# Kernel tuning notes

Measured on AMD Instinct MI355X. Metric: run time of the kernel, lower is better.

## Reference

```python
import jax, jax.numpy as jnp
import numpy as np
from jax import lax

V, E, H, D = 50000, 300, 128, 128   # vocab, embed, gru_units, dense_units
B, S, W, T = 32, 512, 20, 16        # batch, sentences/doc, words/sentence, topics/doc


def setup_inputs() -> dict:
    key = jax.random.key(0)
    ks = jax.random.split(key, 16)
    word_ids = jax.random.randint(ks[0], (B, S, W), 0, V, dtype=jnp.int32)
    # contiguous equal topic segments, 1-based inclusive boundaries
    L = S // T
    starts = (1 + np.arange(T) * L).astype(np.int32)
    ends = (starts + L - 1).astype(np.int32)
    topic_start_ends = jnp.asarray(np.broadcast_to(np.stack([starts, ends], -1), (B, T, 2)))
    sc = 0.05
    def rn(k, shape, s=sc):
        return jax.random.normal(k, shape, dtype=jnp.float32) * s
    inp = {
        "word_ids": word_ids,
        "topic_start_ends": topic_start_ends,
        "emb": rn(ks[1], (V, E), 0.6),
        "Wih_f": rn(ks[2], (3 * H, E)), "Whh_f": rn(ks[3], (3 * H, H)),
        "bih_f": rn(ks[4], (3 * H,)),   "bhh_f": rn(ks[5], (3 * H,)),
        "Wih_b": rn(ks[6], (3 * H, E)), "Whh_b": rn(ks[7], (3 * H, H)),
        "bih_b": rn(ks[8], (3 * H,)),   "bhh_b": rn(ks[9], (3 * H,)),
        "W_att": rn(ks[10], (4 * H, 4 * H)), "v_att": rn(ks[11], (4 * H, 1)),
        "W1": rn(ks[12], (D, 4 * H)), "b1": rn(ks[13], (D,)),
        "W2": rn(ks[14], (1, D)),     "b2": rn(ks[15], (1,)),
    }
    return inp


def _gru_dir(x_sbe, Wih, Whh, bih, bhh, reverse):
    """x_sbe: [S,B,E] -> (outputs [S,B,H] in original time order, last hidden [B,H])."""
    h0 = jnp.zeros((x_sbe.shape[1], Whh.shape[1]), x_sbe.dtype)
    def step(h, xt):
        gx = xt @ Wih.T + bih            # [B,3H]
        gh = h @ Whh.T + bhh
        xr, xz, xn = jnp.split(gx, 3, axis=-1)   # PyTorch gate order: r,z,n
        hr, hz, hn = jnp.split(gh, 3, axis=-1)
        r = jax.nn.sigmoid(xr + hr)
        z = jax.nn.sigmoid(xz + hz)
        n = jnp.tanh(xn + r * hn)
        h2 = (1.0 - z) * n + z * h
        return h2, h2
    last, outs = lax.scan(step, h0, x_sbe, reverse=reverse)
    return outs, last


def reference(word_ids, topic_start_ends, emb,
              Wih_f, Whh_f, bih_f, bhh_f,
              Wih_b, Whh_b, bih_b, bhh_b,
              W_att, v_att, W1, b1, W2, b2):
    # --- sent_encoder: mean word embedding per sentence ---
    x = jnp.mean(emb[word_ids], axis=2)              # [B,S,E]
    # --- doc_encoder: biGRU over sentences ---
    xs = jnp.swapaxes(x, 0, 1)                       # [S,B,E]
    out_f, last_f = _gru_dir(xs, Wih_f, Whh_f, bih_f, bhh_f, reverse=False)
    out_b, last_b = _gru_dir(xs, Wih_b, Whh_b, bih_b, bhh_b, reverse=True)
    sent_rep = jnp.swapaxes(jnp.concatenate([out_f, out_b], axis=-1), 0, 1)  # [B,S,2H]
    # faithful to torch hidden.view(B, 2H) on [2,B,H] contiguous memory
    doc_vec = jnp.stack([last_f, last_b], axis=0).reshape(sent_rep.shape[0], 2 * last_f.shape[1])
    doc_rep = jnp.broadcast_to(doc_vec[:, None, :], sent_rep.shape)          # [B,S,2H]
    # --- topic segment extraction via boundary diffs on zero-padded GRU out ---
    Bn, Sn, twoH = sent_rep.shape
    Hn = twoH // 2
    P = jnp.pad(sent_rep, ((0, 0), (1, 1), (0, 0)))   # [B,S+2,2H]; index i = 1-based sentence i
    starts = topic_start_ends[..., 0]                 # [B,T], 1-based
    ends = topic_start_ends[..., 1]
    bidx = jnp.arange(Bn)[:, None]
    fw = P[bidx, ends, :Hn] - P[bidx, starts - 1, :Hn]      # forward-dir diff
    bw = P[bidx, starts, Hn:] - P[bidx, ends + 1, Hn:]      # backward-dir diff
    topic_mat = jnp.concatenate([fw, bw], axis=-1)          # [B,T,2H]
    # scatter: sentence s (0-based) belongs to topic with starts-1 <= s <= ends-1
    pos = jnp.arange(Sn, dtype=starts.dtype) + 1            # 1-based sentence ids
    seg = jax.vmap(lambda st: jnp.searchsorted(st, pos, side='right') - 1)(starts)  # [B,S]
    topic_rep = jnp.take_along_axis(topic_mat, seg[..., None], axis=1)              # [B,S,2H]
    # --- decoder ---
    cat_ds = jnp.concatenate([doc_rep, sent_rep], axis=-1)   # [B,S,4H]
    cat_ts = jnp.concatenate([topic_rep, sent_rep], axis=-1)
    doc_scores = jnp.tanh(cat_ds @ W_att) @ v_att            # [B,S,1]
    topic_scores = jnp.tanh(cat_ts @ W_att) @ v_att
    ssum = doc_scores + topic_scores
    context = (doc_scores / ssum) * doc_rep + (topic_scores / ssum) * topic_rep
    inp = jnp.concatenate([sent_rep, context], axis=-1)      # [B,S,4H]
    h = jax.nn.relu(inp @ W1.T + b1)                         # dropout = identity (eval)
    logits = h @ W2.T + b2                                   # [B,S,1]
    return logits
```

## Files before the change

kernel.cpp:

```cpp
#include <hip/hip_runtime.h>
#include <hip/hip_bf16.h>

#define B_ 32
#define S_ 512
#define W_ 20
#define T_ 16
#define E_ 300
#define H_ 128
#define M_ (B_*S_)

#define OFF_GX        0ul
#define OFF_X         12582912ul
#define OFF_SENT      17498112ul
#define OFF_LASTF     21692416ul
#define OFF_LASTB     21696512ul
#define OFF_DOCVEC    21700608ul
#define OFF_TOPICMAT  21708800ul
#define OFF_DOCPART   21839872ul
#define OFF_TOPICPART 21856256ul
#define OFF_SEG       22118400ul
#define OFF_WTIH      22134784ul
#define OFF_BIASIH    22365184ul
#define OFF_W1T       22365952ul
#define OFF_H         22431488ul
#define OFF_SRPART    0ul
#define OFF_CTX       OFF_X

__global__ void prep_kernel(const float* __restrict__ Wih_f, const float* __restrict__ Wih_b,
                            const float* __restrict__ bih_f, const float* __restrict__ bih_b,
                            const float* __restrict__ W1,
                            float* __restrict__ Wt_ih, float* __restrict__ bias_ih,
                            float* __restrict__ W1t) {
  int idx = blockIdx.x * 256 + threadIdx.x;
  if (idx < E_ * 768) {
    int k = idx / 768, g = idx % 768;
    Wt_ih[idx] = (g < 384) ? Wih_f[g * E_ + k] : Wih_b[(g - 384) * E_ + k];
  }
  if (idx < 768) bias_ih[idx] = (idx < 384) ? bih_f[idx] : bih_b[idx - 384];
  if (idx < 512 * 128) { int k = idx / 128, j = idx % 128; W1t[idx] = W1[j * 512 + k]; }
}

__global__ void embed_mean_kernel(const int* __restrict__ wid, const float* __restrict__ emb,
                                  float* __restrict__ x) {
  int m = blockIdx.x;
  const int* ids = wid + (size_t)m * W_;
  int e = threadIdx.x;
  float s0 = 0.f, s1 = 0.f, s2 = 0.f;
  for (int w = 0; w < W_; w++) {
    const float* row = emb + (size_t)ids[w] * E_;
    s0 += row[e];
    s1 += row[e + 128];
    if (e < E_ - 256) s2 += row[e + 256];
  }
  const float inv = 1.0f / (float)W_;
  float* xr = x + (size_t)m * E_;
  xr[e] = s0 * inv; xr[e + 128] = s1 * inv; if (e < E_ - 256) xr[e + 256] = s2 * inv;
}

template<bool BIAS, bool ACCUM, bool RELU>
__global__ __launch_bounds__(256) void gemm64(
    const float* __restrict__ A, int lda,
    const float* __restrict__ B, int ldb,
    float* __restrict__ C, int ldc,
    const float* __restrict__ bias,
    int M, int N, int K) {
  __shared__ float As[16][68];
  __shared__ float Bs[16][68];
  const int tid = threadIdx.x;
  const int n0 = blockIdx.x * 64, m0 = blockIdx.y * 64;
  const int tx = tid & 15, ty = tid >> 4;
  const int am = tid >> 2, ak = (tid & 3) << 2;
  const int bk = tid >> 4, bn = (tid & 15) << 2;
  float acc[4][4] = {};
  for (int k0 = 0; k0 < K; k0 += 16) {
    float4 av = make_float4(0.f, 0.f, 0.f, 0.f);
    int arow = m0 + am;
    if (arow < M) {
      if (k0 + ak + 3 < K) {
        av = *(const float4*)(A + (size_t)arow * lda + k0 + ak);
      } else {
        float tmp[4] = {0.f, 0.f, 0.f, 0.f};
        #pragma unroll
        for (int i2 = 0; i2 < 4; i2++) { int k = k0 + ak + i2; if (k < K) tmp[i2] = A[(size_t)arow * lda + k]; }
        av = make_float4(tmp[0], tmp[1], tmp[2], tmp[3]);
      }
    }
    As[ak + 0][am] = av.x; As[ak + 1][am] = av.y; As[ak + 2][am] = av.z; As[ak + 3][am] = av.w;
    float4 bv = make_float4(0.f, 0.f, 0.f, 0.f);
    {
      int k = k0 + bk;
      if (k < K) bv = *(const float4*)(B + (size_t)k * ldb + n0 + bn);
    }
    *(float4*)&Bs[bk][bn] = bv;
    __syncthreads();
    #pragma unroll
    for (int kk = 0; kk < 16; kk++) {
      float4 a = *(const float4*)&As[kk][ty << 2];
      float4 b = *(const float4*)&Bs[kk][tx << 2];
      acc[0][0] = fmaf(a.x, b.x, acc[0][0]); acc[0][1] = fmaf(a.x, b.y, acc[0][1]);
      acc[0][2] = fmaf(a.x, b.z, acc[0][2]); acc[0][3] = fmaf(a.x, b.w, acc[0][3]);
      acc[1][0] = fmaf(a.y, b.x, acc[1][0]); acc[1][1] = fmaf(a.y, b.y, acc[1][1]);
      acc[1][2] = fmaf(a.y, b.z, acc[1][2]); acc[1][3] = fmaf(a.y, b.w, acc[1][3]);
      acc[2][0] = fmaf(a.z, b.x, acc[2][0]); acc[2][1] = fmaf(a.z, b.y, acc[2][1]);
      acc[2][2] = fmaf(a.z, b.z, acc[2][2]); acc[2][3] = fmaf(a.z, b.w, acc[2][3]);
      acc[3][0] = fmaf(a.w, b.x, acc[3][0]); acc[3][1] = fmaf(a.w, b.y, acc[3][1]);
      acc[3][2] = fmaf(a.w, b.z, acc[3][2]); acc[3][3] = fmaf(a.w, b.w, acc[3][3]);
    }
    __syncthreads();
  }
  float4 bias4 = make_float4(0.f, 0.f, 0.f, 0.f);
  if (BIAS) bias4 = *(const float4*)(bias + n0 + (tx << 2));
  #pragma unroll
  for (int i = 0; i < 4; i++) {
    int row = m0 + (ty << 2) + i;
    if (row >= M) break;
    float* cp = C + (size_t)row * ldc + n0 + (tx << 2);
    float4 v = make_float4(acc[i][0], acc[i][1], acc[i][2], acc[i][3]);
    if (BIAS) { v.x += bias4.x; v.y += bias4.y; v.z += bias4.z; v.w += bias4.w; }
    if (ACCUM) { float4 o = *(const float4*)cp; v.x += o.x; v.y += o.y; v.z += o.z; v.w += o.w; }
    if (RELU) { v.x = fmaxf(v.x, 0.f); v.y = fmaxf(v.y, 0.f); v.z = fmaxf(v.z, 0.f); v.w = fmaxf(v.w, 0.f); }
    *(float4*)cp = v;
  }
}

__global__ __launch_bounds__(384, 2) void gru_kernel(
    const float* __restrict__ gxbuf,
    const float* __restrict__ Whh_f, const float* __restrict__ Whh_b,
    const float* __restrict__ bhh_f, const float* __restrict__ bhh_b,
    float* __restrict__ sent_rep,
    float* __restrict__ last_f, float* __restrict__ last_b) {
  int bid = blockIdx.x;
  int dir = bid >> 5, b = bid & 31;
  int g = threadIdx.x;
  const float* Whh = dir ? Whh_b : Whh_f;
  const float* bhh = dir ? bhh_b : bhh_f;
  float4 w[32];
  #pragma unroll
  for (int kk = 0; kk < 32; kk++) w[kk] = *(const float4*)(Whh + (size_t)g * 128 + kk * 4);
  float bh = bhh[g];
  __shared__ float h_lds[128];
  __shared__ float r_lds[128];
  __shared__ float z_lds[128];
  if (g < 128) h_lds[g] = 0.f;
  __syncthreads();
  int j = g - 256;
  const float* gx0 = gxbuf + (size_t)b * 512 * 768 + dir * 384 + g;
  int ts = dir ? 511 : 0;
  int step = dir ? -1 : 1;
  float* srow = sent_rep + (size_t)b * 512 * 256 + dir * 128;
  float gx_c = gx0[(size_t)ts * 768];
  float gx_n1 = gx0[(size_t)(ts + step) * 768];
  for (int s = 0; s < 512; s++) {
    float gx_n2 = 0.f;
    if (s + 2 < 512) gx_n2 = gx0[(size_t)(ts + 2 * step) * 768];
    float4 acc4 = make_float4(0.f, 0.f, 0.f, 0.f);
    const float4* h4 = (const float4*)h_lds;
    #pragma unroll
    for (int kk = 0; kk < 32; kk++) {
      float4 hv = h4[kk];
      acc4.x = fmaf(w[kk].x, hv.x, acc4.x);
      acc4.y = fmaf(w[kk].y, hv.y, acc4.y);
      acc4.z = fmaf(w[kk].z, hv.z, acc4.z);
      acc4.w = fmaf(w[kk].w, hv.w, acc4.w);
    }
    float hdot = (acc4.x + acc4.y) + (acc4.z + acc4.w) + bh;
    if (g < 256) {
      float pre = gx_c + hdot;
      float sg_ = 1.f / (1.f + expf(-pre));
      if (g < 128) r_lds[g] = sg_; else z_lds[g - 128] = sg_;
    }
    __syncthreads();
    if (g >= 256) {
      float r = r_lds[j];
      float nval = tanhf(gx_c + r * hdot);
      float z = z_lds[j];
      float hold = h_lds[j];
      float hnew = (1.f - z) * nval + z * hold;
      h_lds[j] = hnew;
      srow[(size_t)ts * 256 + j] = hnew;
    }
    __syncthreads();
    ts += step;
    gx_c = gx_n1; gx_n1 = gx_n2;
  }
  if (g < 128) (dir ? last_b : last_f)[b * 128 + g] = h_lds[g];
}

__global__ void docvec_kernel(const float* __restrict__ last_f, const float* __restrict__ last_b,
                              float* __restrict__ doc_vec) {
  int idx = blockIdx.x * 256 + threadIdx.x;
  int i = idx >> 8, c = idx & 255;
  const float* src = (i < 16) ? last_f : last_b;
  int ii = (i < 16) ? i : i - 16;
  int bb = 2 * ii + (c >> 7);
  doc_vec[idx] = src[bb * 128 + (c & 127)];
}

__global__ void topicmat_kernel(const float* __restrict__ sent_rep, const int* __restrict__ tse,
                                float* __restrict__ topic_mat) {
  int bt = blockIdx.x;
  int b = bt >> 4, t = bt & 15;
  int st = tse[(b * 16 + t) * 2 + 0];
  int en = tse[(b * 16 + t) * 2 + 1];
  int jj = threadIdx.x;
  const float* sr = sent_rep + (size_t)b * 512 * 256;
  float val;
  if (jj < 128) {
    float a = sr[(size_t)(en - 1) * 256 + jj];
    float c = (st - 2 >= 0) ? sr[(size_t)(st - 2) * 256 + jj] : 0.f;
    val = a - c;
  } else {
    float a = sr[(size_t)(st - 1) * 256 + jj];
    float c = (en <= 511) ? sr[(size_t)en * 256 + jj] : 0.f;
    val = a - c;
  }
  topic_mat[(size_t)bt * 256 + jj] = val;
}

__global__ void seg_kernel(const int* __restrict__ tse, int* __restrict__ seg) {
  int idx = blockIdx.x * 256 + threadIdx.x;
  int b = idx >> 9, s = idx & 511;
  int pos = s + 1, cnt = 0;
  for (int t = 0; t < T_; t++) cnt += (tse[(b * T_ + t) * 2] <= pos);
  int sg = cnt - 1; sg = sg < 0 ? 0 : (sg > T_ - 1 ? T_ - 1 : sg);
  seg[idx] = sg;
}

__global__ void scores_ctx_kernel(const float* __restrict__ sr_part,
                                  const float* __restrict__ doc_part,
                                  const float* __restrict__ topic_part,
                                  const float* __restrict__ v_att,
                                  const float* __restrict__ doc_vec,
                                  const float* __restrict__ topic_mat,
                                  const int* __restrict__ seg,
                                  float* __restrict__ context) {
  int wid = threadIdx.x >> 6, lane = threadIdx.x & 63;
  int row = blockIdx.x * 4 + wid;
  int b = row >> 9;
  int sg = seg[row];
  const float* srp = sr_part + (size_t)row * 512;
  const float* dp = doc_part + (size_t)b * 512;
  const float* tp = topic_part + (size_t)(b * 16 + sg) * 512;
  float accd = 0.f, acct = 0.f;
  #pragma unroll
  for (int i = 0; i < 8; i++) {
    int n = lane + i * 64;
    float sp = srp[n], va = v_att[n];
    accd += tanhf(dp[n] + sp) * va;
    acct += tanhf(tp[n] + sp) * va;
  }
  #pragma unroll
  for (int off = 32; off; off >>= 1) { accd += __shfl_xor(accd, off); acct += __shfl_xor(acct, off); }
  float ssum = accd + acct;
  float rd = accd / ssum, rt = acct / ssum;
  const float* dv = doc_vec + (size_t)b * 256;
  const float* tm = topic_mat + (size_t)(b * 16 + sg) * 256;
  float* ctx = context + (size_t)row * 256;
  #pragma unroll
  for (int i = 0; i < 4; i++) {
    int jj = lane + i * 64;
    ctx[jj] = rd * dv[jj] + rt * tm[jj];
  }
}

__global__ void logits_kernel(const float* __restrict__ h, const float* __restrict__ W2,
                              const float* __restrict__ b2, float* __restrict__ out, int M) {
  int wid = threadIdx.x >> 6, lane = threadIdx.x & 63;
  int row = blockIdx.x * 4 + wid;
  if (row >= M) return;
  const float* hp = h + (size_t)row * 128;
  float s = hp[lane] * W2[lane] + hp[lane + 64] * W2[lane + 64];
  #pragma unroll
  for (int off = 32; off; off >>= 1) s += __shfl_xor(s, off);
  if (lane == 0) out[row] = s + b2[0];
}

extern "C" void kernel_launch(void* const* d_in, const int* in_sizes, int n_in,
                              void* d_out, int out_size, void* d_ws, size_t ws_size,
                              hipStream_t stream) {
  const int*   word_ids = (const int*)d_in[0];
  const int*   tse      = (const int*)d_in[1];
  const float* emb      = (const float*)d_in[2];
  const float* Wih_f    = (const float*)d_in[3];
  const float* Whh_f    = (const float*)d_in[4];
  const float* bih_f    = (const float*)d_in[5];
  const float* bhh_f    = (const float*)d_in[6];
  const float* Wih_b    = (const float*)d_in[7];
  const float* Whh_b    = (const float*)d_in[8];
  const float* bih_b    = (const float*)d_in[9];
  const float* bhh_b    = (const float*)d_in[10];
  const float* W_att    = (const float*)d_in[11];
  const float* v_att    = (const float*)d_in[12];
  const float* W1       = (const float*)d_in[13];
  const float* b1       = (const float*)d_in[14];
  const float* W2       = (const float*)d_in[15];
  const float* b2       = (const float*)d_in[16];
  float* ws  = (float*)d_ws;
  float* out = (float*)d_out;

  prep_kernel<<<900, 256, 0, stream>>>(Wih_f, Wih_b, bih_f, bih_b, W1,
                                       ws + OFF_WTIH, ws + OFF_BIASIH, ws + OFF_W1T);
  embed_mean_kernel<<<M_, 128, 0, stream>>>(word_ids, emb, ws + OFF_X);
  gemm64<true, false, false><<<dim3(12, 256), 256, 0, stream>>>(
      ws + OFF_X, E_, ws + OFF_WTIH, 768, ws + OFF_GX, 768, ws + OFF_BIASIH, M_, 768, E_);
  gru_kernel<<<64, 384, 0, stream>>>(ws + OFF_GX, Whh_f, Whh_b, bhh_f, bhh_b,
                                     ws + OFF_SENT, ws + OFF_LASTF, ws + OFF_LASTB);
  docvec_kernel<<<32, 256, 0, stream>>>(ws + OFF_LASTF, ws + OFF_LASTB, ws + OFF_DOCVEC);
  topicmat_kernel<<<512, 256, 0, stream>>>(ws + OFF_SENT, tse, ws + OFF_TOPICMAT);
  seg_kernel<<<64, 256, 0, stream>>>(tse, (int*)(ws + OFF_SEG));
  gemm64<false, false, false><<<dim3(8, 1), 256, 0, stream>>>(
      ws + OFF_DOCVEC, 256, W_att, 512, ws + OFF_DOCPART, 512, nullptr, 32, 512, 256);
  gemm64<false, false, false><<<dim3(8, 8), 256, 0, stream>>>(
      ws + OFF_TOPICMAT, 256, W_att, 512, ws + OFF_TOPICPART, 512, nullptr, 512, 512, 256);
  gemm64<false, false, false><<<dim3(8, 256), 256, 0, stream>>>(
      ws + OFF_SENT, 256, W_att + 256 * 512, 512, ws + OFF_SRPART, 512, nullptr, M_, 512, 256);
  scores_ctx_kernel<<<M_ / 4, 256, 0, stream>>>(
      ws + OFF_SRPART, ws + OFF_DOCPART, ws + OFF_TOPICPART, v_att,
      ws + OFF_DOCVEC, ws + OFF_TOPICMAT, (const int*)(ws + OFF_SEG), ws + OFF_CTX);
  gemm64<true, false, false><<<dim3(2, 256), 256, 0, stream>>>(
      ws + OFF_SENT, 256, ws + OFF_W1T, 128, ws + OFF_H, 128, b1, M_, 128, 256);
  gemm64<false, true, true><<<dim3(2, 256), 256, 0, stream>>>(
      ws + OFF_CTX, 256, ws + OFF_W1T + 256 * 128, 128, ws + OFF_H, 128, nullptr, M_, 128, 256);
  logits_kernel<<<M_ / 4, 256, 0, stream>>>(ws + OFF_H, W2, b2, out, M_);
}
```

Before: 842.7 us.

## Restructure GRU recurrence as split-K across waves with readlane hidden-state broadcast

The GRU recurrent kernel now uses 256 threads per block. Each thread computes all three gates for one hidden unit over half of the K dimension, taking h values from registers via readlane broadcasts instead of reading them from LDS. Owner threads keep h in a register, add the partial sums from the other half, and apply the gate nonlinearities. This removes LDS reads of h from the inner loop and shortens the serial path per timestep, at the cost of 192 weight registers per thread and a partial-sum exchange through shared memory.

```diff
diff --git a/kernel.cpp b/kernel.cpp
--- a/kernel.cpp
+++ b/kernel.cpp
@@ -123,67 +123,88 @@
   }
 }
 
-__global__ __launch_bounds__(384, 2) void gru_kernel(
+__global__ __launch_bounds__(256, 1) void gru_kernel(
     const float* __restrict__ gxbuf,
     const float* __restrict__ Whh_f, const float* __restrict__ Whh_b,
     const float* __restrict__ bhh_f, const float* __restrict__ bhh_b,
     float* __restrict__ sent_rep,
     float* __restrict__ last_f, float* __restrict__ last_b) {
-  int bid = blockIdx.x;
-  int dir = bid >> 5, b = bid & 31;
-  int g = threadIdx.x;
+  const int bid = blockIdx.x;
+  const int dir = bid >> 5, b = bid & 31;
+  const int t = threadIdx.x;
+  const int j = t & 127;
+  const int lane = t & 63;
+  const int q = ((t >> 6) ^ (t >> 7)) & 1;
+  const int k0 = q << 6;
+  const bool owner = (t < 128);
   const float* Whh = dir ? Whh_b : Whh_f;
   const float* bhh = dir ? bhh_b : bhh_f;
-  float4 w[32];
-  #pragma unroll
-  for (int kk = 0; kk < 32; kk++) w[kk] = *(const float4*)(Whh + (size_t)g * 128 + kk * 4);
-  float bh = bhh[g];
-  __shared__ float h_lds[128];
-  __shared__ float r_lds[128];
-  __shared__ float z_lds[128];
-  if (g < 128) h_lds[g] = 0.f;
+
+  float wr[64], wz[64], wn[64];
+  #pragma unroll
+  for (int kk = 0; kk < 64; kk += 4) {
+    float4 a = *(const float4*)(Whh + (size_t)j * 128 + k0 + kk);
+    wr[kk] = a.x; wr[kk + 1] = a.y; wr[kk + 2] = a.z; wr[kk + 3] = a.w;
+    float4 c = *(const float4*)(Whh + (size_t)(128 + j) * 128 + k0 + kk);
+    wz[kk] = c.x; wz[kk + 1] = c.y; wz[kk + 2] = c.z; wz[kk + 3] = c.w;
+    float4 d = *(const float4*)(Whh + (size_t)(256 + j) * 128 + k0 + kk);
+    wn[kk] = d.x; wn[kk + 1] = d.y; wn[kk + 2] = d.z; wn[kk + 3] = d.w;
+  }
+  float bhr = 0.f, bhz = 0.f, bhn = 0.f;
+  if (owner) { bhr = bhh[j]; bhz = bhh[128 + j]; bhn = bhh[256 + j]; }
+
+  __shared__ float hbuf[128];
+  __shared__ float rp[128], zp[128], np_[128];
+  if (t < 128) hbuf[t] = 0.f;
   __syncthreads();
-  int j = g - 256;
-  const float* gx0 = gxbuf + (size_t)b * 512 * 768 + dir * 384 + g;
+
+  float hown = 0.f;
+  const float* gx0 = gxbuf + (size_t)b * 512 * 768 + dir * 384 + j;
   int ts = dir ? 511 : 0;
-  int step = dir ? -1 : 1;
+  const int stp = dir ? -1 : 1;
   float* srow = sent_rep + (size_t)b * 512 * 256 + dir * 128;
-  float gx_c = gx0[(size_t)ts * 768];
-  float gx_n1 = gx0[(size_t)(ts + step) * 768];
+
+  float gr_c = 0.f, gz_c = 0.f, gn_c = 0.f, gr_1 = 0.f, gz_1 = 0.f, gn_1 = 0.f;
+  if (owner) {
+    const float* p0 = gx0 + (size_t)ts * 768;
+    gr_c = p0[0]; gz_c = p0[128]; gn_c = p0[256];
+    const float* p1 = gx0 + (size_t)(ts + stp) * 768;
+    gr_1 = p1[0]; gz_1 = p1[128]; gn_1 = p1[256];
+  }
+
   for (int s = 0; s < 512; s++) {
-    float gx_n2 = 0.f;
-    if (s + 2 < 512) gx_n2 = gx0[(size_t)(ts + 2 * step) * 768];
-    float4 acc4 = make_float4(0.f, 0.f, 0.f, 0.f);
-    const float4* h4 = (const float4*)h_lds;
+    float gr_2 = 0.f, gz_2 = 0.f, gn_2 = 0.f;
+    if (owner && s + 2 < 512) {
+      const float* p2 = gx0 + (size_t)(ts + 2 * stp) * 768;
+      gr_2 = p2[0]; gz_2 = p2[128]; gn_2 = p2[256];
+    }
+    float hreg = owner ? hown : hbuf[k0 + lane];
+    float ar = 0.f, az = 0.f, an = 0.f;
     #pragma unroll
-    for (int kk = 0; kk < 32; kk++) {
-      float4 hv = h4[kk];
-      acc4.x = fmaf(w[kk].x, hv.x, acc4.x);
-      acc4.y = fmaf(w[kk].y, hv.y, acc4.y);
-      acc4.z = fmaf(w[kk].z, hv.z, acc4.z);
-      acc4.w = fmaf(w[kk].w, hv.w, acc4.w);
-    }
-    float hdot = (acc4.x + acc4.y) + (acc4.z + acc4.w) + bh;
-    if (g < 256) {
-      float pre = gx_c + hdot;
-      float sg_ = 1.f / (1.f + expf(-pre));
-      if (g < 128) r_lds[g] = sg_; else z_lds[g - 128] = sg_;
-    }
+    for (int kk = 0; kk < 64; kk++) {
+      float hv = __int_as_float(__builtin_amdgcn_readlane(__float_as_int(hreg), kk));
+      ar = fmaf(wr[kk], hv, ar);
+      az = fmaf(wz[kk], hv, az);
+      an = fmaf(wn[kk], hv, an);
+    }
+    if (!owner) { rp[j] = ar; zp[j] = az; np_[j] = an; }
     __syncthreads();
-    if (g >= 256) {
-      float r = r_lds[j];
-      float nval = tanhf(gx_c + r * hdot);
-      float z = z_lds[j];
-      float hold = h_lds[j];
-      float hnew = (1.f - z) * nval + z * hold;
-      h_lds[j] = hnew;
+    if (owner) {
+      ar += rp[j]; az += zp[j]; an += np_[j];
+      float r = 1.f / (1.f + expf(-(gr_c + ar + bhr)));
+      float z = 1.f / (1.f + expf(-(gz_c + az + bhz)));
+      float n = tanhf(gn_c + r * (an + bhn));
+      float hnew = (1.f - z) * n + z * hown;
+      hown = hnew;
+      hbuf[j] = hnew;
       srow[(size_t)ts * 256 + j] = hnew;
     }
     __syncthreads();
-    ts += step;
-    gx_c = gx_n1; gx_n1 = gx_n2;
-  }
-  if (g < 128) (dir ? last_b : last_f)[b * 128 + g] = h_lds[g];
+    ts += stp;
+    gr_c = gr_1; gz_c = gz_1; gn_c = gn_1;
+    gr_1 = gr_2; gz_1 = gz_2; gn_1 = gn_2;
+  }
+  if (owner) (dir ? last_b : last_f)[b * 128 + j] = hown;
 }
 
 __global__ void docvec_kernel(const float* __restrict__ last_f, const float* __restrict__ last_b,
@@ -303,7 +324,7 @@
   embed_mean_kernel<<<M_, 128, 0, stream>>>(word_ids, emb, ws + OFF_X);
   gemm64<true, false, false><<<dim3(12, 256), 256, 0, stream>>>(
       ws + OFF_X, E_, ws + OFF_WTIH, 768, ws + OFF_GX, 768, ws + OFF_BIASIH, M_, 768, E_);
-  gru_kernel<<<64, 384, 0, stream>>>(ws + OFF_GX, Whh_f, Whh_b, bhh_f, bhh_b,
+  gru_kernel<<<64, 256, 0, stream>>>(ws + OFF_GX, Whh_f, Whh_b, bhh_f, bhh_b,
                                      ws + OFF_SENT, ws + OFF_LASTF, ws + OFF_LASTB);
   docvec_kernel<<<32, 256, 0, stream>>>(ws + OFF_LASTF, ws + OFF_LASTB, ws + OFF_DOCVEC);
   topicmat_kernel<<<512, 256, 0, stream>>>(ws + OFF_SENT, tse, ws + OFF_TOPICMAT);
```

New measurement: 935.3 us. +11.0%, slower.

## Restructure GRU recurrence into split-K wave layout with one barrier per step

Applied to the files above, without the earlier changes.

The GRU recurrence kernel now uses 512 threads per block. Each hidden unit's r, z and n dot products are split across four 16-lane groups, each covering 32 of the 128 inputs, and the partial sums are combined with cross-lane shuffles. This lets each thread compute all three gates for its unit in registers, and double-buffering the hidden state in LDS cuts the per-step barriers from two to one. The serial 512-step loop is the critical path, so removing a barrier and the LDS round trips for r and z should shorten each step, at the cost of shuffle reductions and tighter register pressure from the pinned weights.

```diff
diff --git a/kernel.cpp b/kernel.cpp
--- a/kernel.cpp
+++ b/kernel.cpp
@@ -123,67 +123,89 @@
   }
 }
 
-__global__ __launch_bounds__(384, 2) void gru_kernel(
+#define PIN4(v) asm volatile("" : "+v"((v).x), "+v"((v).y), "+v"((v).z), "+v"((v).w))
+__global__ __launch_bounds__(512) __attribute__((amdgpu_waves_per_eu(2, 2)))
+void gru_kernel(
     const float* __restrict__ gxbuf,
     const float* __restrict__ Whh_f, const float* __restrict__ Whh_b,
     const float* __restrict__ bhh_f, const float* __restrict__ bhh_b,
     float* __restrict__ sent_rep,
     float* __restrict__ last_f, float* __restrict__ last_b) {
-  int bid = blockIdx.x;
-  int dir = bid >> 5, b = bid & 31;
-  int g = threadIdx.x;
+  const int bid = blockIdx.x;
+  const int dir = bid >> 5, b = bid & 31;
+  const int t = threadIdx.x;
+  const int wave = t >> 6;
+  const int lane = t & 63;
+  const int q = lane >> 4;
+  const int j = (wave << 4) + (lane & 15);
+  const int k0 = q << 5;
   const float* Whh = dir ? Whh_b : Whh_f;
   const float* bhh = dir ? bhh_b : bhh_f;
-  float4 w[32];
-  #pragma unroll
-  for (int kk = 0; kk < 32; kk++) w[kk] = *(const float4*)(Whh + (size_t)g * 128 + kk * 4);
-  float bh = bhh[g];
-  __shared__ float h_lds[128];
-  __shared__ float r_lds[128];
-  __shared__ float z_lds[128];
-  if (g < 128) h_lds[g] = 0.f;
+
+  float4 wr4[8], wz4[8], wn4[8];
+  #pragma unroll
+  for (int i = 0; i < 8; i++) {
+    wr4[i] = *(const float4*)(Whh + (size_t)j * 128 + k0 + i * 4);
+    wz4[i] = *(const float4*)(Whh + (size_t)(128 + j) * 128 + k0 + i * 4);
+    wn4[i] = *(const float4*)(Whh + (size_t)(256 + j) * 128 + k0 + i * 4);
+  }
+  #pragma unroll
+  for (int i = 0; i < 8; i++) { PIN4(wr4[i]); PIN4(wz4[i]); PIN4(wn4[i]); }
+
+  const float bhr = bhh[j], bhz = bhh[128 + j], bhn = bhh[256 + j];
+  const int gate = q ? (q - 1) : 2;
+  const float mr = (q == 1) ? 1.f : 0.f;
+  const float mz = (q == 2) ? 1.f : 0.f;
+  const float* gxp = gxbuf + (size_t)b * 512 * 768 + dir * 384 + gate * 128 + j;
+
+  __shared__ float hbuf[2][128];
+  if (t < 128) hbuf[0][t] = 0.f;
   __syncthreads();
-  int j = g - 256;
-  const float* gx0 = gxbuf + (size_t)b * 512 * 768 + dir * 384 + g;
+
+  float hprev = 0.f;
   int ts = dir ? 511 : 0;
-  int step = dir ? -1 : 1;
+  const int stp = dir ? -1 : 1;
   float* srow = sent_rep + (size_t)b * 512 * 256 + dir * 128;
-  float gx_c = gx0[(size_t)ts * 768];
-  float gx_n1 = gx0[(size_t)(ts + step) * 768];
+
+  float gx_c = gxp[(size_t)ts * 768];
+  float gx_1 = gxp[(size_t)(ts + stp) * 768];
+
+  #pragma unroll 1
   for (int s = 0; s < 512; s++) {
-    float gx_n2 = 0.f;
-    if (s + 2 < 512) gx_n2 = gx0[(size_t)(ts + 2 * step) * 768];
-    float4 acc4 = make_float4(0.f, 0.f, 0.f, 0.f);
-    const float4* h4 = (const float4*)h_lds;
+    float gx_2 = 0.f;
+    if (s + 2 < 512) gx_2 = gxp[(size_t)(ts + 2 * stp) * 768];
+    const float4* h4 = (const float4*)(&hbuf[s & 1][k0]);
+    float pr = 0.f, pz = 0.f, pn = 0.f;
     #pragma unroll
-    for (int kk = 0; kk < 32; kk++) {
-      float4 hv = h4[kk];
-      acc4.x = fmaf(w[kk].x, hv.x, acc4.x);
-      acc4.y = fmaf(w[kk].y, hv.y, acc4.y);
-      acc4.z = fmaf(w[kk].z, hv.z, acc4.z);
-      acc4.w = fmaf(w[kk].w, hv.w, acc4.w);
-    }
-    float hdot = (acc4.x + acc4.y) + (acc4.z + acc4.w) + bh;
-    if (g < 256) {
-      float pre = gx_c + hdot;
-      float sg_ = 1.f / (1.f + expf(-pre));
-      if (g < 128) r_lds[g] = sg_; else z_lds[g - 128] = sg_;
+    for (int i = 0; i < 8; i++) {
+      float4 hv = h4[i];
+      pr = fmaf(wr4[i].x, hv.x, pr); pr = fmaf(wr4[i].y, hv.y, pr);
+      pr = fmaf(wr4[i].z, hv.z, pr); pr = fmaf(wr4[i].w, hv.w, pr);
+      pz = fmaf(wz4[i].x, hv.x, pz); pz = fmaf(wz4[i].y, hv.y, pz);
+      pz = fmaf(wz4[i].z, hv.z, pz); pz = fmaf(wz4[i].w, hv.w, pz);
+      pn = fmaf(wn4[i].x, hv.x, pn); pn = fmaf(wn4[i].y, hv.y, pn);
+      pn = fmaf(wn4[i].z, hv.z, pn); pn = fmaf(wn4[i].w, hv.w, pn);
+    }
+    pr = fmaf(mr, gx_c, pr);
+    pz = fmaf(mz, gx_c, pz);
+    pr += __shfl_xor(pr, 16); pr += __shfl_xor(pr, 32);
+    pz += __shfl_xor(pz, 16); pz += __shfl_xor(pz, 32);
+    pn += __shfl_xor(pn, 16); pn += __shfl_xor(pn, 32);
+    float gn = __shfl(gx_c, (lane & 15) + 48);
+    float r = 1.f / (1.f + expf(-(pr + bhr)));
+    float z = 1.f / (1.f + expf(-(pz + bhz)));
+    float n = tanhf(gn + r * (pn + bhn));
+    float hnew = (1.f - z) * n + z * hprev;
+    hprev = hnew;
+    if (q == 0) {
+      hbuf[(s + 1) & 1][j] = hnew;
+      srow[(size_t)ts * 256 + j] = hnew;
     }
     __syncthreads();
-    if (g >= 256) {
-      float r = r_lds[j];
-      float nval = tanhf(gx_c + r * hdot);
-      float z = z_lds[j];
-      float hold = h_lds[j];
-      float hnew = (1.f - z) * nval + z * hold;
-      h_lds[j] = hnew;
-      srow[(size_t)ts * 256 + j] = hnew;
-    }
-    __syncthreads();
-    ts += step;
-    gx_c = gx_n1; gx_n1 = gx_n2;
-  }
-  if (g < 128) (dir ? last_b : last_f)[b * 128 + g] = h_lds[g];
+    ts += stp;
+    gx_c = gx_1; gx_1 = gx_2;
+  }
+  if (q == 0) (dir ? last_b : last_f)[b * 128 + j] = hprev;
 }
 
 __global__ void docvec_kernel(const float* __restrict__ last_f, const float* __restrict__ last_b,
@@ -303,7 +325,7 @@
   embed_mean_kernel<<<M_, 128, 0, stream>>>(word_ids, emb, ws + OFF_X);
   gemm64<true, false, false><<<dim3(12, 256), 256, 0, stream>>>(
       ws + OFF_X, E_, ws + OFF_WTIH, 768, ws + OFF_GX, 768, ws + OFF_BIASIH, M_, 768, E_);
-  gru_kernel<<<64, 384, 0, stream>>>(ws + OFF_GX, Whh_f, Whh_b, bhh_f, bhh_b,
+  gru_kernel<<<64, 512, 0, stream>>>(ws + OFF_GX, Whh_f, Whh_b, bhh_f, bhh_b,
                                      ws + OFF_SENT, ws + OFF_LASTF, ws + OFF_LASTB);
   docvec_kernel<<<32, 256, 0, stream>>>(ws + OFF_LASTF, ws + OFF_LASTB, ws + OFF_DOCVEC);
   topicmat_kernel<<<512, 256, 0, stream>>>(ws + OFF_SENT, tse, ws + OFF_TOPICMAT);
```

New measurement: 733.7 us. 12.9% less time.
